# Kernel optimization log

Measured on AMD Instinct MI355X. Metric: run time of the kernel, lower is better.

## Reference

```python
import jax, jax.numpy as jnp
import numpy as np

NEG_SLOPE = 0.2  # PyG GATConv default LeakyReLU negative slope


def gat_conv(x, src, dst, W, att_src, att_dst, bias, heads, out_ch, concat):
    """PyG-style GATConv (eval mode, self-loops already appended to src/dst)."""
    n = x.shape[0]
    xh = (x @ W).reshape(n, heads, out_ch)          # [N, H, C]
    a_src = jnp.sum(xh * att_src, axis=-1)          # [N, H]
    a_dst = jnp.sum(xh * att_dst, axis=-1)          # [N, H]
    e = jax.nn.leaky_relu(a_src[src] + a_dst[dst], NEG_SLOPE)  # [E, H]
    # segment softmax over edges grouped by destination node
    m = jax.ops.segment_max(e, dst, num_segments=n)
    m = jnp.where(jnp.isfinite(m), m, 0.0)
    ex = jnp.exp(e - m[dst])
    denom = jax.ops.segment_sum(ex, dst, num_segments=n)
    alpha = ex / (denom[dst] + 1e-16)               # [E, H]
    msg = xh[src] * alpha[..., None]                # [E, H, C]
    out = jax.ops.segment_sum(msg, dst, num_segments=n)  # [N, H, C]
    out = out.reshape(n, heads * out_ch) if concat else out.mean(axis=1)
    return out + bias


def setup_inputs() -> dict:
    key = jax.random.key(0)
    ks = jax.random.split(key, 10)
    N, E, IN, OUT = 50000, 600000, 128, 64
    H1, C1 = 2, 2 * OUT   # conv1: heads=2, out=2*out_channels, concat -> 4*OUT
    H2, C2 = 1, OUT       # conv2: heads=1, concat=False
    s = 0.05
    return {
        "x": jax.random.normal(ks[0], (N, IN), dtype=jnp.float32),
        "edge_index": jax.random.randint(ks[1], (2, E), 0, N, dtype=jnp.int64),
        "W1": jax.random.normal(ks[2], (IN, H1 * C1), dtype=jnp.float32) * s,
        "att_src1": jax.random.normal(ks[3], (H1, C1), dtype=jnp.float32) * s,
        "att_dst1": jax.random.normal(ks[4], (H1, C1), dtype=jnp.float32) * s,
        "b1": jnp.zeros((H1 * C1,), dtype=jnp.float32),
        "W2": jax.random.normal(ks[5], (H1 * C1, H2 * C2), dtype=jnp.float32) * s,
        "att_src2": jax.random.normal(ks[6], (H2, C2), dtype=jnp.float32) * s,
        "att_dst2": jax.random.normal(ks[7], (H2, C2), dtype=jnp.float32) * s,
        "b2": jnp.zeros((C2,), dtype=jnp.float32),
    }


def reference(x, edge_index, W1, att_src1, att_dst1, b1, W2, att_src2, att_dst2, b2):
    n = x.shape[0]
    loop = jnp.arange(n, dtype=edge_index.dtype)
    src = jnp.concatenate([edge_index[0], loop])  # add_self_loops=True
    dst = jnp.concatenate([edge_index[1], loop])
    z = gat_conv(x, src, dst, W1, att_src1, att_dst1, b1, heads=2, out_ch=128, concat=True)
    z = jax.nn.relu(z)
    z = gat_conv(z, src, dst, W2, att_src2, att_dst2, b2, heads=1, out_ch=64, concat=False)
    # decode: dot product over original edge_index (no self loops)
    val = jnp.sum(z[edge_index[0]] * z[edge_index[1]], axis=-1)
    return val.reshape(-1)
```

## Files before the change

### kernel.cpp

```cpp
#include <hip/hip_runtime.h>
#include <math.h>

#define IN_F 128
#define F1 256
#define H1 2
#define F2 64
#define NEG 0.2f

template<int KTOT, int TM, int TN, int RM, int RN, int LDA, int LDW, int LDC,
         bool RELU, bool ATT_EP, bool HEADOFF>
__global__ __launch_bounds__(256) void gemm_tiled(
    const float* __restrict__ A, const float* __restrict__ bias,
    const float* __restrict__ W, float* __restrict__ C,
    const float* __restrict__ att_s, const float* __restrict__ att_d,
    float* __restrict__ a_src, float* __restrict__ a_dst, int M)
{
    constexpr int NX = TN / RN;
    constexpr int NY = 256 / NX;
    static_assert(NY * RM == TM, "tile mismatch");
    static_assert(RN == 8, "split-col mapping assumes RN==8");
    __shared__ float As[32][TM];
    __shared__ float Ws[32][TN];
    int t = threadIdx.x;
    int tx = t % NX, ty = t / NX;
    int m0 = blockIdx.x * TM;
    int n0 = blockIdx.y * TN;
    long aoff = HEADOFF ? (long)blockIdx.y * KTOT : 0;
    float acc[RM][RN];
    #pragma unroll
    for (int i = 0; i < RM; ++i)
        #pragma unroll
        for (int j = 0; j < RN; ++j) acc[i][j] = 0.f;

    constexpr int PARTS = 256 / TM;
    constexpr int F4PT = 8 / PARTS;
    int ar = t % TM, apart = t / TM;
    int arow = m0 + ar; if (arow >= M) arow = M - 1;
    constexpr int WTPK = TN / 4;
    constexpr int WKP = 256 / WTPK;
    int wk0 = t / WTPK, wc = t % WTPK;

    for (int kc = 0; kc < KTOT; kc += 32) {
        const float* ap = A + (long)arow * LDA + aoff + kc + apart * (F4PT * 4);
        #pragma unroll
        for (int p = 0; p < F4PT; ++p) {
            int kk = apart * (F4PT * 4) + p * 4;
            float4 v = *(const float4*)(ap + p * 4);
            if (RELU) {
                float4 bb = *(const float4*)&bias[kc + kk];
                v.x = fmaxf(v.x + bb.x, 0.f);
                v.y = fmaxf(v.y + bb.y, 0.f);
                v.z = fmaxf(v.z + bb.z, 0.f);
                v.w = fmaxf(v.w + bb.w, 0.f);
            }
            As[kk + 0][ar] = v.x;
            As[kk + 1][ar] = v.y;
            As[kk + 2][ar] = v.z;
            As[kk + 3][ar] = v.w;
        }
        #pragma unroll
        for (int p = 0; p < 32 / WKP; ++p) {
            int k = wk0 + p * WKP;
            *(float4*)&Ws[k][wc * 4] =
                *(const float4*)&W[(long)(kc + k) * LDW + n0 + wc * 4];
        }
        __syncthreads();
        #pragma unroll 4
        for (int k = 0; k < 32; ++k) {
            float av[RM], wv[RN];
            #pragma unroll
            for (int i4 = 0; i4 < RM / 4; ++i4) {
                float4 v = *(const float4*)&As[k][ty * RM + i4 * 4];
                av[i4 * 4 + 0] = v.x; av[i4 * 4 + 1] = v.y;
                av[i4 * 4 + 2] = v.z; av[i4 * 4 + 3] = v.w;
            }
            {
                float4 v = *(const float4*)&Ws[k][tx * 4];
                wv[0] = v.x; wv[1] = v.y; wv[2] = v.z; wv[3] = v.w;
                float4 u = *(const float4*)&Ws[k][TN / 2 + tx * 4];
                wv[4] = u.x; wv[5] = u.y; wv[6] = u.z; wv[7] = u.w;
            }
            #pragma unroll
            for (int i = 0; i < RM; ++i)
                #pragma unroll
                for (int j = 0; j < RN; ++j)
                    acc[i][j] = fmaf(av[i], wv[j], acc[i][j]);
        }
        __syncthreads();
    }
    #pragma unroll
    for (int i = 0; i < RM; ++i) {
        int row = m0 + ty * RM + i;
        if (row < M) {
            float4 o0 = {acc[i][0], acc[i][1], acc[i][2], acc[i][3]};
            float4 o1 = {acc[i][4], acc[i][5], acc[i][6], acc[i][7]};
            *(float4*)&C[(long)row * LDC + n0 + tx * 4] = o0;
            *(float4*)&C[(long)row * LDC + n0 + TN / 2 + tx * 4] = o1;
        }
    }
    if (ATT_EP) {
        float asr[RN], adr[RN];
        #pragma unroll
        for (int j = 0; j < RN; ++j) {
            int col = (j < 4) ? (tx * 4 + j) : (TN / 2 + tx * 4 + j - 4);
            asr[j] = att_s[col];
            adr[j] = att_d[col];
        }
        #pragma unroll
        for (int i = 0; i < RM; ++i) {
            float ps = 0.f, pd = 0.f;
            #pragma unroll
            for (int j = 0; j < RN; ++j) {
                ps = fmaf(acc[i][j], asr[j], ps);
                pd = fmaf(acc[i][j], adr[j], pd);
            }
            #pragma unroll
            for (int o = 1; o < NX; o <<= 1) {
                ps += __shfl_xor(ps, o);
                pd += __shfl_xor(pd, o);
            }
            int row = m0 + ty * RM + i;
            if (tx == 0 && row < M) { a_src[row] = ps; a_dst[row] = pd; }
        }
    }
}

__global__ __launch_bounds__(256) void hist_uv_k(
    const int* __restrict__ ei_d, int* __restrict__ deg, int* __restrict__ pos,
    int E, int Ep, int NBH,
    const float* __restrict__ W1, const float* __restrict__ as1,
    const float* __restrict__ ad1, float* __restrict__ UV4)
{
    if ((int)blockIdx.x < NBH) {
        int i = blockIdx.x * 256 + threadIdx.x;
        if (i >= Ep) return;
        int d = (i < E) ? ei_d[i] : (i - E);
        pos[i] = atomicAdd(&deg[d], 1);
    } else {
        int t = threadIdx.x;
        int k = t >> 1, h = t & 1;
        const float* wrow = W1 + (long)k * F1 + h * 128;
        const float* sa = as1 + h * 128;
        const float* da = ad1 + h * 128;
        float u = 0.f, v = 0.f;
        for (int c = 0; c < 128; ++c) {
            float w = wrow[c];
            u = fmaf(w, sa[c], u);
            v = fmaf(w, da[c], v);
        }
        UV4[k * 4 + h] = u;
        UV4[k * 4 + 2 + h] = v;
    }
}

__global__ __launch_bounds__(1024) void scanA_att_k(
    const int* __restrict__ deg, int* __restrict__ rowptr, int* __restrict__ bsum,
    int N, int NBLK,
    const float* __restrict__ x, const float* __restrict__ UV4,
    float* __restrict__ a_src, float* __restrict__ a_dst)
{
    if ((int)blockIdx.x < NBLK) {
        __shared__ int wsum[16];
        int t = threadIdx.x, lane = t & 63, w = t >> 6;
        int i = blockIdx.x * 1024 + t;
        int v = (i < N) ? deg[i] : 0;
        int incl = v;
        #pragma unroll
        for (int o = 1; o < 64; o <<= 1) {
            int nb = __shfl_up(incl, o);
            if (lane >= o) incl += nb;
        }
        if (lane == 63) wsum[w] = incl;
        __syncthreads();
        if (w == 0 && lane < 16) {
            int s = wsum[lane];
            #pragma unroll
            for (int o = 1; o < 16; o <<= 1) {
                int nb = __shfl_up(s, o);
                if (lane >= o) s += nb;
            }
            wsum[lane] = s;
        }
        __syncthreads();
        int woff = (w == 0) ? 0 : wsum[w - 1];
        if (i < N) rowptr[i] = woff + incl - v;
        if (t == 1023) bsum[blockIdx.x] = woff + incl;
    } else {
        int wave = threadIdx.x >> 6, lane = threadIdx.x & 63;
        int n = ((int)blockIdx.x - NBLK) * 16 + wave;
        if (n >= N) return;
        float2 xv = ((const float2*)(x + (long)n * IN_F))[lane];
        float4 u0 = ((const float4*)UV4)[2 * lane];
        float4 u1 = ((const float4*)UV4)[2 * lane + 1];
        float p0 = xv.x * u0.x + xv.y * u1.x;
        float p1 = xv.x * u0.y + xv.y * u1.y;
        float p2 = xv.x * u0.z + xv.y * u1.z;
        float p3 = xv.x * u0.w + xv.y * u1.w;
        #pragma unroll
        for (int o = 32; o > 0; o >>= 1) {
            p0 += __shfl_xor(p0, o); p1 += __shfl_xor(p1, o);
            p2 += __shfl_xor(p2, o); p3 += __shfl_xor(p3, o);
        }
        if (lane == 0) {
            a_src[(long)n * 2 + 0] = p0; a_src[(long)n * 2 + 1] = p1;
            a_dst[(long)n * 2 + 0] = p2; a_dst[(long)n * 2 + 1] = p3;
        }
    }
}

__global__ __launch_bounds__(1024) void scanC2_k(
    int* __restrict__ rowptr, const int* __restrict__ bsum, int NBLK, int N)
{
    __shared__ int bex_sh, tot_sh;
    int t = threadIdx.x;
    if (t < 64) {
        int lane = t;
        int v = (lane < NBLK) ? bsum[lane] : 0;
        int incl = v;
        #pragma unroll
        for (int o = 1; o < 64; o <<= 1) {
            int nb = __shfl_up(incl, o);
            if (lane >= o) incl += nb;
        }
        if (lane == (int)blockIdx.x) bex_sh = incl - v;
        if (lane == NBLK - 1) tot_sh = incl;
    }
    __syncthreads();
    int i = blockIdx.x * 1024 + t;
    if (i < N) rowptr[i] += bex_sh;
    if ((int)blockIdx.x == NBLK - 1 && t == 0) rowptr[N] = tot_sh;
}

__global__ void scatter_nc(const int* __restrict__ ei_s, const int* __restrict__ ei_d,
                           const int* __restrict__ rowptr, const int* __restrict__ pos,
                           int* __restrict__ csr_src, int* __restrict__ csr_eid,
                           int E, int Ep)
{
    int i = blockIdx.x * blockDim.x + threadIdx.x;
    if (i >= Ep) return;
    int s = (i < E) ? ei_s[i] : (i - E);
    int d = (i < E) ? ei_d[i] : (i - E);
    int at = rowptr[d] + pos[i];
    csr_src[at] = s;
    csr_eid[at] = (i < E) ? i : -1;
}

__global__ __launch_bounds__(256) void agg1x(
    const int* __restrict__ rowptr, const int* __restrict__ csr_src,
    const float* __restrict__ a_s, const float* __restrict__ a_d,
    const float* __restrict__ x, float* __restrict__ G, int N)
{
    int wave = threadIdx.x >> 6, lane = threadIdx.x & 63;
    int d = blockIdx.x * 4 + wave;
    if (d >= N) return;
    int row = rowptr[d], end = rowptr[d + 1];
    int h = lane >> 5, l5 = lane & 31;
    float adh = a_d[(long)d * 2 + h];
    float a0[4] = {0,0,0,0}, a1[4] = {0,0,0,0};
    float den = 0.f;
    for (int base = row; base < end; base += 32) {
        int cnt = min(32, end - base);
        int sreg = 0; float e = 0.f;
        if (l5 < cnt) {
            sreg = csr_src[base + l5];
            float v = a_s[(long)sreg * 2 + h] + adh;
            v = (v > 0.f) ? v : NEG * v;
            e = expf(v);
            den += e;
        }
        int jmax = (cnt + 1) >> 1;
        for (int j = 0; j < jmax; ++j) {
            int m = 2 * j + h;
            int s = __shfl(sreg, m);
            float w0 = __shfl(e, m);
            float w1 = __shfl(e, 32 | m);
            float4 v = *(const float4*)(x + (long)s * IN_F + l5 * 4);
            a0[0] = fmaf(w0, v.x, a0[0]); a0[1] = fmaf(w0, v.y, a0[1]);
            a0[2] = fmaf(w0, v.z, a0[2]); a0[3] = fmaf(w0, v.w, a0[3]);
            a1[0] = fmaf(w1, v.x, a1[0]); a1[1] = fmaf(w1, v.y, a1[1]);
            a1[2] = fmaf(w1, v.z, a1[2]); a1[3] = fmaf(w1, v.w, a1[3]);
        }
    }
    #pragma unroll
    for (int o = 16; o > 0; o >>= 1) den += __shfl_xor(den, o);
    #pragma unroll
    for (int p = 0; p < 4; ++p) {
        a0[p] += __shfl_xor(a0[p], 32);
        a1[p] += __shfl_xor(a1[p], 32);
    }
    float inv = 1.0f / (den + 1e-16f);
    float* acch = (h == 0) ? a0 : a1;
    float4 o4 = {acch[0] * inv, acch[1] * inv, acch[2] * inv, acch[3] * inv};
    *(float4*)(G + (long)d * F1 + h * 128 + l5 * 4) = o4;
}

__global__ __launch_bounds__(256) void agg2_csr(
    const int* __restrict__ rowptr, const int* __restrict__ csr_src,
    const float* __restrict__ a_s, const float* __restrict__ a_d,
    const float* __restrict__ xh2, const float* __restrict__ b2,
    float* __restrict__ out2b, int N)
{
    int wave = threadIdx.x >> 6, lane = threadIdx.x & 63;
    int d = blockIdx.x * 4 + wave;
    if (d >= N) return;
    int row = rowptr[d], end = rowptr[d + 1];
    float adv = a_d[d];
    int g = lane >> 4, q = lane & 15;
    float acc[4] = {0,0,0,0};
    float den = 0.f;
    for (int base = row; base < end; base += 64) {
        int cnt = min(64, end - base);
        float ev = 0.f; int sreg = 0;
        if (lane < cnt) {
            sreg = csr_src[base + lane];
            float v = a_s[sreg] + adv; v = (v > 0.f) ? v : NEG * v;
            ev = expf(v);
            den += ev;
        }
        int jmax = (cnt + 3) >> 2;
        for (int j = 0; j < jmax; ++j) {
            int m = 4 * j + g;
            int s = __shfl(sreg, m);
            float w = __shfl(ev, m);
            float4 v = *(const float4*)(xh2 + (long)s * F2 + q * 4);
            acc[0] = fmaf(w, v.x, acc[0]); acc[1] = fmaf(w, v.y, acc[1]);
            acc[2] = fmaf(w, v.z, acc[2]); acc[3] = fmaf(w, v.w, acc[3]);
        }
    }
    #pragma unroll
    for (int o = 32; o > 0; o >>= 1) den += __shfl_xor(den, o);
    #pragma unroll
    for (int p = 0; p < 4; ++p) {
        acc[p] += __shfl_xor(acc[p], 16);
        acc[p] += __shfl_xor(acc[p], 32);
    }
    if (g == 0) {
        float inv = 1.0f / (den + 1e-16f);
        float4 bb = *(const float4*)&b2[q * 4];
        float4 o4 = {acc[0] * inv + bb.x, acc[1] * inv + bb.y,
                     acc[2] * inv + bb.z, acc[3] * inv + bb.w};
        *(float4*)(out2b + (long)d * F2 + q * 4) = o4;
    }
}

__global__ __launch_bounds__(256) void decode_csr(
    const int* __restrict__ rowptr, const int* __restrict__ csr_src,
    const int* __restrict__ csr_eid, const float* __restrict__ z2b,
    float* __restrict__ out, int N)
{
    int wave = threadIdx.x >> 6, lane = threadIdx.x & 63;
    int d = blockIdx.x * 4 + wave;
    if (d >= N) return;
    int row = rowptr[d], end = rowptr[d + 1];
    int g = lane >> 4, q = lane & 15;
    float4 vd = *(const float4*)(z2b + (long)d * F2 + q * 4);
    for (int base = row; base < end; base += 64) {
        int cnt = min(64, end - base);
        int sreg = 0, ereg = -1;
        if (lane < cnt) {
            sreg = csr_src[base + lane];
            ereg = csr_eid[base + lane];
        }
        int jmax = (cnt + 3) >> 2;
        for (int j = 0; j < jmax; ++j) {
            int m = 4 * j + g;
            int s = __shfl(sreg, m);
            int eid = __shfl(ereg, m);
            float4 vs = *(const float4*)(z2b + (long)s * F2 + q * 4);
            float p = vd.x * vs.x + vd.y * vs.y + vd.z * vs.z + vd.w * vs.w;
            #pragma unroll
            for (int o = 1; o < 16; o <<= 1) p += __shfl_xor(p, o);
            if (q == 0 && eid >= 0) out[eid] = p;
        }
    }
}

extern "C" void kernel_launch(void* const* d_in, const int* in_sizes, int n_in,
                              void* d_out, int out_size, void* d_ws, size_t ws_size,
                              hipStream_t stream) {
    const float* x   = (const float*)d_in[0];
    const int*   ei  = (const int*)d_in[1];
    const float* W1  = (const float*)d_in[2];
    const float* as1 = (const float*)d_in[3];
    const float* ad1 = (const float*)d_in[4];
    const float* b1  = (const float*)d_in[5];
    const float* W2  = (const float*)d_in[6];
    const float* as2 = (const float*)d_in[7];
    const float* ad2 = (const float*)d_in[8];
    const float* b2  = (const float*)d_in[9];

    int N  = in_sizes[0] / IN_F;
    int E  = in_sizes[1] / 2;
    int Ep = E + N;
    const int* ei_src = ei;
    const int* ei_dst = ei + E;

    float* ws = (float*)d_ws;
    size_t off = 0;
    auto alloc = [&](size_t n) { float* p = ws + off; off += (n + 63) & ~(size_t)63; return p; };

    float* G      = alloc((size_t)N * F1);
    float* z1     = alloc((size_t)N * F1);
    float* xh2    = alloc((size_t)N * F2);
    float* out2b  = alloc((size_t)N * F2);
    float* a_src1 = alloc((size_t)N * H1);
    float* a_dst1 = alloc((size_t)N * H1);
    float* a_src2 = alloc(N);
    float* a_dst2 = alloc(N);
    float* UV4    = alloc(IN_F * 4);
    int* rowptr   = (int*)alloc(N + 64);
    int* csr_src  = (int*)alloc(Ep);
    int* csr_eid  = (int*)alloc(Ep);
    int* pos      = (int*)alloc(Ep);
    int* bsum     = (int*)alloc(64);
    int* deg      = (int*)alloc(N);
    hipMemsetAsync(deg, 0, (size_t)N * sizeof(int), stream);

    int NBLK = (N + 1023) / 1024;
    int NBH  = (Ep + 255) / 256;
    int NBA  = (N + 15) / 16;

    hist_uv_k<<<NBH + 1, 256, 0, stream>>>(ei_dst, deg, pos, E, Ep, NBH,
                                           W1, as1, ad1, UV4);
    scanA_att_k<<<NBLK + NBA, 1024, 0, stream>>>(deg, rowptr, bsum, N, NBLK,
                                                 x, UV4, a_src1, a_dst1);
    scanC2_k<<<NBLK, 1024, 0, stream>>>(rowptr, bsum, NBLK, N);
    scatter_nc<<<NBH, 256, 0, stream>>>(ei_src, ei_dst, rowptr, pos,
                                        csr_src, csr_eid, E, Ep);

    agg1x<<<(N + 3) / 4, 256, 0, stream>>>(rowptr, csr_src, a_src1, a_dst1, x, G, N);
    int mt1 = (N + 127) / 128;
    gemm_tiled<IN_F, 128, 128, 8, 8, F1, F1, F1, false, false, true>
        <<<dim3(mt1, 2), 256, 0, stream>>>(
        G, nullptr, W1, z1, nullptr, nullptr, nullptr, nullptr, N);

    gemm_tiled<F1, 128, 64, 4, 8, F1, F2, F2, true, true, false>
        <<<dim3(mt1, 1), 256, 0, stream>>>(
        z1, b1, W2, xh2, as2, ad2, a_src2, a_dst2, N);
    agg2_csr<<<(N + 3) / 4, 256, 0, stream>>>(rowptr, csr_src, a_src2, a_dst2, xh2, b2, out2b, N);

    decode_csr<<<(N + 3) / 4, 256, 0, stream>>>(rowptr, csr_src, csr_eid, out2b,
                                                (float*)d_out, N);
}
```

Before: 348.4 us.

## Stage full weight tile in LDS and stream A rows from global with prefetch

The GEMM kernel now loads the entire K x TN weight slice into shared memory once per block, and no longer tiles A through LDS. Each thread instead reads its own rows of A directly from global memory as float4 along K, with a one-step register prefetch. This removes the per-K-chunk A staging, the transposed LDS writes and the per-chunk barriers. In exchange each thread issues strided, uncoalesced global reads of A with no reuse across threads, and LDS usage grows to 64KB for the first GEMM, which may lower occupancy.

```diff
diff --git a/kernel.cpp b/kernel.cpp
--- a/kernel.cpp
+++ b/kernel.cpp
@@ -9,7 +9,7 @@
 
 template<int KTOT, int TM, int TN, int RM, int RN, int LDA, int LDW, int LDC,
          bool RELU, bool ATT_EP, bool HEADOFF>
-__global__ __launch_bounds__(256) void gemm_tiled(
+__global__ __launch_bounds__(256) void gemm_wlds(
     const float* __restrict__ A, const float* __restrict__ bias,
     const float* __restrict__ W, float* __restrict__ C,
     const float* __restrict__ att_s, const float* __restrict__ att_d,
@@ -19,61 +19,60 @@
     constexpr int NY = 256 / NX;
     static_assert(NY * RM == TM, "tile mismatch");
     static_assert(RN == 8, "split-col mapping assumes RN==8");
-    __shared__ float As[32][TM];
-    __shared__ float Ws[32][TN];
+    __shared__ float Ws[KTOT][TN];
     int t = threadIdx.x;
     int tx = t % NX, ty = t / NX;
     int m0 = blockIdx.x * TM;
     int n0 = blockIdx.y * TN;
     long aoff = HEADOFF ? (long)blockIdx.y * KTOT : 0;
+
+    constexpr int TOT4 = KTOT * TN / 4;
+    #pragma unroll
+    for (int p = 0; p < TOT4 / 256; ++p) {
+        int idx = p * 256 + t;
+        int k = idx / (TN / 4);
+        int c = idx % (TN / 4);
+        *(float4*)&Ws[k][c * 4] = *(const float4*)&W[(long)k * LDW + n0 + c * 4];
+    }
+    __syncthreads();
+
+    const float* ap[RM];
+    #pragma unroll
+    for (int i = 0; i < RM; ++i) {
+        int r = m0 + ty * RM + i;
+        if (r >= M) r = M - 1;
+        ap[i] = A + (long)r * LDA + aoff;
+    }
     float acc[RM][RN];
     #pragma unroll
     for (int i = 0; i < RM; ++i)
         #pragma unroll
         for (int j = 0; j < RN; ++j) acc[i][j] = 0.f;
 
-    constexpr int PARTS = 256 / TM;
-    constexpr int F4PT = 8 / PARTS;
-    int ar = t % TM, apart = t / TM;
-    int arow = m0 + ar; if (arow >= M) arow = M - 1;
-    constexpr int WTPK = TN / 4;
-    constexpr int WKP = 256 / WTPK;
-    int wk0 = t / WTPK, wc = t % WTPK;
-
-    for (int kc = 0; kc < KTOT; kc += 32) {
-        const float* ap = A + (long)arow * LDA + aoff + kc + apart * (F4PT * 4);
-        #pragma unroll
-        for (int p = 0; p < F4PT; ++p) {
-            int kk = apart * (F4PT * 4) + p * 4;
-            float4 v = *(const float4*)(ap + p * 4);
-            if (RELU) {
-                float4 bb = *(const float4*)&bias[kc + kk];
-                v.x = fmaxf(v.x + bb.x, 0.f);
-                v.y = fmaxf(v.y + bb.y, 0.f);
-                v.z = fmaxf(v.z + bb.z, 0.f);
-                v.w = fmaxf(v.w + bb.w, 0.f);
-            }
-            As[kk + 0][ar] = v.x;
-            As[kk + 1][ar] = v.y;
-            As[kk + 2][ar] = v.z;
-            As[kk + 3][ar] = v.w;
-        }
-        #pragma unroll
-        for (int p = 0; p < 32 / WKP; ++p) {
-            int k = wk0 + p * WKP;
-            *(float4*)&Ws[k][wc * 4] =
-                *(const float4*)&W[(long)(kc + k) * LDW + n0 + wc * 4];
-        }
-        __syncthreads();
-        #pragma unroll 4
-        for (int k = 0; k < 32; ++k) {
-            float av[RM], wv[RN];
-            #pragma unroll
-            for (int i4 = 0; i4 < RM / 4; ++i4) {
-                float4 v = *(const float4*)&As[k][ty * RM + i4 * 4];
-                av[i4 * 4 + 0] = v.x; av[i4 * 4 + 1] = v.y;
-                av[i4 * 4 + 2] = v.z; av[i4 * 4 + 3] = v.w;
-            }
+    float4 cur[RM], nxt[RM];
+    #pragma unroll
+    for (int i = 0; i < RM; ++i) cur[i] = *(const float4*)(ap[i]);
+
+    for (int kq = 0; kq < KTOT / 4; ++kq) {
+        if (kq + 1 < KTOT / 4) {
+            #pragma unroll
+            for (int i = 0; i < RM; ++i)
+                nxt[i] = *(const float4*)(ap[i] + (kq + 1) * 4);
+        }
+        if (RELU) {
+            float4 bq = *(const float4*)&bias[kq * 4];
+            #pragma unroll
+            for (int i = 0; i < RM; ++i) {
+                cur[i].x = fmaxf(cur[i].x + bq.x, 0.f);
+                cur[i].y = fmaxf(cur[i].y + bq.y, 0.f);
+                cur[i].z = fmaxf(cur[i].z + bq.z, 0.f);
+                cur[i].w = fmaxf(cur[i].w + bq.w, 0.f);
+            }
+        }
+        #pragma unroll
+        for (int kk = 0; kk < 4; ++kk) {
+            int k = kq * 4 + kk;
+            float wv[RN];
             {
                 float4 v = *(const float4*)&Ws[k][tx * 4];
                 wv[0] = v.x; wv[1] = v.y; wv[2] = v.z; wv[3] = v.w;
@@ -81,13 +80,18 @@
                 wv[4] = u.x; wv[5] = u.y; wv[6] = u.z; wv[7] = u.w;
             }
             #pragma unroll
-            for (int i = 0; i < RM; ++i)
+            for (int i = 0; i < RM; ++i) {
+                const float* cf = (const float*)&cur[i];
+                float a = cf[kk];
                 #pragma unroll
                 for (int j = 0; j < RN; ++j)
-                    acc[i][j] = fmaf(av[i], wv[j], acc[i][j]);
-        }
-        __syncthreads();
-    }
+                    acc[i][j] = fmaf(a, wv[j], acc[i][j]);
+            }
+        }
+        #pragma unroll
+        for (int i = 0; i < RM; ++i) cur[i] = nxt[i];
+    }
+
     #pragma unroll
     for (int i = 0; i < RM; ++i) {
         int row = m0 + ty * RM + i;
@@ -430,11 +434,11 @@
 
     agg1x<<<(N + 3) / 4, 256, 0, stream>>>(rowptr, csr_src, a_src1, a_dst1, x, G, N);
     int mt1 = (N + 127) / 128;
-    gemm_tiled<IN_F, 128, 128, 8, 8, F1, F1, F1, false, false, true>
+    gemm_wlds<IN_F, 128, 128, 8, 8, F1, F1, F1, false, false, true>
         <<<dim3(mt1, 2), 256, 0, stream>>>(
         G, nullptr, W1, z1, nullptr, nullptr, nullptr, nullptr, N);
 
-    gemm_tiled<F1, 128, 64, 4, 8, F1, F2, F2, true, true, false>
+    gemm_wlds<F1, 128, 64, 4, 8, F1, F2, F2, true, true, false>
         <<<dim3(mt1, 1), 256, 0, stream>>>(
         z1, b1, W2, xh2, as2, ad2, a_src2, a_dst2, N);
     agg2_csr<<<(N + 3) / 4, 256, 0, stream>>>(rowptr, csr_src, a_src2, a_dst2, xh2, b2, out2b, N);
```

Result: no change. 346.0 us (-0.7%).
